# Performance work log

Measured on AMD Instinct MI355X. Metric: run time of the kernel, lower is better.

Reference implementation:

```python
import jax, jax.numpy as jnp
import numpy as np

N_NODES = 100000


def _mean_aggregate(h, src, dst, inv_deg):
    # gather source-node features per edge, scatter-add into dst, divide by in-degree
    summed = jax.ops.segment_sum(h[src], dst, num_segments=N_NODES)  # [N, d]
    return summed * inv_deg[:, None]


def setup_inputs() -> dict:
    key = jax.random.key(0)
    ks = jax.random.split(key, 6)
    n_edges, d = 640000, 128
    h = jax.random.normal(ks[0], (N_NODES, d), dtype=jnp.float32)
    src = jax.random.randint(ks[1], (n_edges,), 0, N_NODES, dtype=jnp.int64)
    dst = jax.random.randint(ks[2], (n_edges,), 0, N_NODES, dtype=jnp.int64)
    W_self = jax.random.normal(ks[3], (3, d, d), dtype=jnp.float32) / np.sqrt(d)
    W_neigh = jax.random.normal(ks[4], (3, d, d), dtype=jnp.float32) / np.sqrt(d)
    b = jnp.zeros((3, d), dtype=jnp.float32)
    return {"h": h, "src": src, "dst": dst, "W_self": W_self, "W_neigh": W_neigh, "b": b}


def reference(h, src, dst, W_self, W_neigh, b):
    # in-degree with clamp to 1 (isolated nodes aggregate to zero)
    deg = jax.ops.segment_sum(jnp.ones_like(src, dtype=h.dtype), dst, num_segments=N_NODES)
    inv_deg = 1.0 / jnp.maximum(deg, 1.0)
    n_layers = W_self.shape[0]
    for i in range(n_layers):
        neigh = _mean_aggregate(h, src, dst, inv_deg)
        h = h @ W_self[i] + neigh @ W_neigh[i] + b[i]
        if i < n_layers - 1:
            h = jax.nn.relu(h)  # dropout p=0 / eval: no-op
    return h
```

## Files before the change

kernel.cpp:

```cpp
#include <hip/hip_runtime.h>
#include <cstdint>
#include <cstddef>

#define NN 100000
#define NPAD 100032
#define D 128
#define K2 256

typedef __attribute__((ext_vector_type(8))) short bf16x8;
typedef __attribute__((ext_vector_type(4))) float f32x4;

__device__ inline float bfhi2f(unsigned int u) {
    union { unsigned int i; float f; } v; v.i = u & 0xffff0000u; return v.f;
}
__device__ inline float bflo2f(unsigned int u) {
    union { unsigned int i; float f; } v; v.i = u << 16; return v.f;
}
__device__ inline unsigned short f2bf(float f) {
    union { float f; unsigned int i; } v; v.f = f;
    unsigned int r = v.i + 0x7FFFu + ((v.i >> 16) & 1u);
    return (unsigned short)(r >> 16);
}

__global__ void k_deg(const int* __restrict__ dst, int ne, int* __restrict__ deg) {
    int e = blockIdx.x * blockDim.x + threadIdx.x;
    if (e < ne) atomicAdd(&deg[dst[e]], 1);
}

__global__ void k_chunk_reduce(const int* __restrict__ deg, int n, int* __restrict__ bsum) {
    __shared__ int s[256];
    int i = blockIdx.x * 256 + threadIdx.x;
    s[threadIdx.x] = (i < n) ? deg[i] : 0;
    __syncthreads();
    for (int off = 128; off > 0; off >>= 1) {
        if (threadIdx.x < off) s[threadIdx.x] += s[threadIdx.x + off];
        __syncthreads();
    }
    if (threadIdx.x == 0) bsum[blockIdx.x] = s[0];
}

__global__ __launch_bounds__(512) void k_scan_partials(int* __restrict__ bsum, int nb,
                                                       int* __restrict__ rowptr, int n) {
    __shared__ int s[512];
    int tid = threadIdx.x;
    int v = (tid < nb) ? bsum[tid] : 0;
    s[tid] = v;
    __syncthreads();
    for (int off = 1; off < 512; off <<= 1) {
        int t = (tid >= off) ? s[tid - off] : 0;
        __syncthreads();
        s[tid] += t;
        __syncthreads();
    }
    if (tid < nb) bsum[tid] = s[tid] - v;
    if (tid == nb - 1) rowptr[n] = s[tid];
}

__global__ void k_chunk_scan(const int* __restrict__ deg, int n, const int* __restrict__ bsum,
                             int* __restrict__ rowptr, int* __restrict__ cursor,
                             float* __restrict__ invd) {
    __shared__ int s[256];
    int tid = threadIdx.x;
    int i = blockIdx.x * 256 + tid;
    int v = (i < n) ? deg[i] : 0;
    s[tid] = v;
    __syncthreads();
    for (int off = 1; off < 256; off <<= 1) {
        int t = (tid >= off) ? s[tid - off] : 0;
        __syncthreads();
        s[tid] += t;
        __syncthreads();
    }
    if (i < n) {
        int excl = bsum[blockIdx.x] + s[tid] - v;
        rowptr[i] = excl;
        cursor[i] = excl;
        invd[i] = 1.0f / fmaxf((float)v, 1.0f);
    }
}

__global__ void k_fill(const int* __restrict__ src, const int* __restrict__ dst, int ne,
                       int* __restrict__ cursor, int* __restrict__ col) {
    int e = blockIdx.x * blockDim.x + threadIdx.x;
    if (e < ne) {
        int p = atomicAdd(&cursor[dst[e]], 1);
        col[p] = src[e];
    }
}

#define T_H   (NN * 32)
#define T_BT  (3 * 128 * K2)
#define T_Z   (NN / 4)
__global__ void k_prep(const float* __restrict__ h, const float* __restrict__ Ws,
                       const float* __restrict__ Wn, unsigned short* __restrict__ Ht,
                       unsigned short* __restrict__ Btf, int4* __restrict__ degz) {
    int t = blockIdx.x * 256 + threadIdx.x;
    if (t < T_H) {
        int row = t >> 5, c4 = (t & 31) << 2;
        float4 v = *(const float4*)(h + (size_t)row * D + c4);
        ushort4 o = make_ushort4(f2bf(v.x), f2bf(v.y), f2bf(v.z), f2bf(v.w));
        *(ushort4*)(Ht + (size_t)row * D + c4) = o;
    } else if (t < T_H + T_BT) {
        int t2 = t - T_H;
        int j = t2 & 7; int rest = t2 >> 3;
        int lane = rest & 63; rest >>= 6;
        int ks = rest & 7; rest >>= 3;
        int nf = rest & 7; int l = rest >> 3;
        int nn = nf * 16 + (lane & 15);
        int k = ks * 32 + (lane >> 4) * 8 + j;
        float v = (k < D) ? Ws[(size_t)l * D * D + (size_t)k * D + nn]
                          : Wn[(size_t)l * D * D + (size_t)(k - D) * D + nn];
        Btf[t2] = f2bf(v);
    } else {
        int t3 = t - T_H - T_BT;
        if (t3 < T_Z) degz[t3] = make_int4(0, 0, 0, 0);
    }
}

__global__ __launch_bounds__(256, 3) void k_layer(const unsigned short* __restrict__ Hin,
                                                  const unsigned short* __restrict__ Btf,
                                                  const float* __restrict__ bias,
                                                  const int* __restrict__ rowptr,
                                                  const int* __restrict__ col,
                                                  const float* __restrict__ invd,
                                                  unsigned short* __restrict__ Hout,
                                                  float* __restrict__ outf,
                                                  int relu) {
    __shared__ unsigned short Ah[64 * 128];
    __shared__ unsigned short An[64 * 128];
    int wid = threadIdx.x >> 6;
    int lane = threadIdx.x & 63;
    int g = lane >> 4;
    int lane16 = lane & 15;
    int m0 = blockIdx.x * 64;

#pragma unroll
    for (int i = 0; i < 4; ++i) {
        int chunk = wid * 4 + i;
        int o = chunk * 1024 + lane * 16;
        int row = o >> 8;
        int cb = o & 255;
        int scb = cb ^ ((row & 7) << 4);
        const unsigned short* gsrc = Hin + (size_t)(m0 + row) * D + (scb >> 1);
        __builtin_amdgcn_global_load_lds(
            (const __attribute__((address_space(1))) unsigned int*)gsrc,
            (__attribute__((address_space(3))) unsigned int*)((char*)Ah + chunk * 1024),
            16, 0, 0);
    }

    int coff = lane16 * 8;
    for (int c = 0; c < 4; ++c) {
        int row = wid * 16 + c * 4 + g;
        int node = m0 + row;
        int e0 = 0, n = 0;
        float inv = 0.f;
        if (node < NN) {
            e0 = rowptr[node];
            n = rowptr[node + 1] - e0;
            inv = invd[node];
        }
        float a0 = 0.f, a1 = 0.f, a2 = 0.f, a3 = 0.f, a4 = 0.f, a5 = 0.f, a6 = 0.f, a7 = 0.f;
        for (int base = 0; base < n; base += 16) {
            int rem = n - base;
            int lim = rem < 16 ? rem : 16;
            int cidx = lane16 < rem ? lane16 : rem - 1;
            int cv = col[e0 + base + cidx];
            for (int j = 0; j < lim; j += 8) {
                uint4 u[8];
#pragma unroll
                for (int k = 0; k < 8; ++k) {
                    int ee = j + k;
                    int eidx = ee < lim ? ee : lim - 1;
                    int si = __shfl(cv, (g << 4) + eidx, 64);
                    u[k] = *(const uint4*)(Hin + (size_t)si * D + coff);
                }
#pragma unroll
                for (int k = 0; k < 8; ++k) {
                    bool live = (j + k) < lim;
                    unsigned int ux = live ? u[k].x : 0u, uy = live ? u[k].y : 0u;
                    unsigned int uz = live ? u[k].z : 0u, uw = live ? u[k].w : 0u;
                    a0 += bflo2f(ux); a1 += bfhi2f(ux);
                    a2 += bflo2f(uy); a3 += bfhi2f(uy);
                    a4 += bflo2f(uz); a5 += bfhi2f(uz);
                    a6 += bflo2f(uw); a7 += bfhi2f(uw);
                }
            }
        }
        uint4 o;
        o.x = ((unsigned int)f2bf(a1 * inv) << 16) | f2bf(a0 * inv);
        o.y = ((unsigned int)f2bf(a3 * inv) << 16) | f2bf(a2 * inv);
        o.z = ((unsigned int)f2bf(a5 * inv) << 16) | f2bf(a4 * inv);
        o.w = ((unsigned int)f2bf(a7 * inv) << 16) | f2bf(a6 * inv);
        int bo = row * 256 + ((lane16 * 16) ^ ((row & 7) << 4));
        *(uint4*)((char*)An + bo) = o;
    }

    bf16x8 bfr[2][8];
#pragma unroll
    for (int q = 0; q < 2; ++q) {
        int nf = wid + q * 4;
#pragma unroll
        for (int ks = 0; ks < 8; ++ks)
            bfr[q][ks] = *(const bf16x8*)(Btf + (size_t)(((nf * 8 + ks) << 6) + lane) * 8);
    }

    __syncthreads();

    f32x4 acc[4][2];
#pragma unroll
    for (int mt = 0; mt < 4; ++mt)
#pragma unroll
        for (int q = 0; q < 2; ++q) acc[mt][q] = (f32x4){0.f, 0.f, 0.f, 0.f};

#pragma unroll
    for (int mt = 0; mt < 4; ++mt) {
        int row = mt * 16 + lane16;
        int swz = (row & 7) << 4;
        bf16x8 a[8];
#pragma unroll
        for (int ks = 0; ks < 8; ++ks) {
            int kb = ks * 64 + g * 16;
            const char* basep = (kb < 256) ? (const char*)Ah : (const char*)An;
            int cb2 = (kb & 255) ^ swz;
            a[ks] = *(const bf16x8*)(basep + row * 256 + cb2);
        }
#pragma unroll
        for (int ks = 0; ks < 8; ++ks) {
            acc[mt][0] = __builtin_amdgcn_mfma_f32_16x16x32_bf16(a[ks], bfr[0][ks], acc[mt][0], 0, 0, 0);
            acc[mt][1] = __builtin_amdgcn_mfma_f32_16x16x32_bf16(a[ks], bfr[1][ks], acc[mt][1], 0, 0, 0);
        }
    }

    float bv[2];
    bv[0] = bias[wid * 16 + lane16];
    bv[1] = bias[(wid + 4) * 16 + lane16];
#pragma unroll
    for (int mt = 0; mt < 4; ++mt) {
#pragma unroll
        for (int q = 0; q < 2; ++q) {
            int colc = (wid + q * 4) * 16 + lane16;
#pragma unroll
            for (int i = 0; i < 4; ++i) {
                int row = m0 + mt * 16 + g * 4 + i;
                if (row >= NN) continue;
                float v = acc[mt][q][i] + bv[q];
                if (relu) v = fmaxf(v, 0.f);
                if (outf) outf[(size_t)row * D + colc] = v;
                else Hout[(size_t)row * D + colc] = f2bf(v);
            }
        }
    }
}

extern "C" void kernel_launch(void* const* d_in, const int* in_sizes, int n_in,
                              void* d_out, int out_size, void* d_ws, size_t ws_size,
                              hipStream_t stream) {
    const float* h = (const float*)d_in[0];
    const int* src = (const int*)d_in[1];
    const int* dst = (const int*)d_in[2];
    const float* Ws = (const float*)d_in[3];
    const float* Wn = (const float*)d_in[4];
    const float* b = (const float*)d_in[5];
    float* out = (float*)d_out;
    int ne = in_sizes[1];

    char* ws = (char*)d_ws;
    unsigned short* HtA = (unsigned short*)ws; ws += (size_t)NPAD * D * sizeof(unsigned short);
    unsigned short* HtB = (unsigned short*)ws; ws += (size_t)NPAD * D * sizeof(unsigned short);
    int* col = (int*)ws;    ws += (size_t)ne * sizeof(int);
    unsigned short* Btf = (unsigned short*)ws; ws += (size_t)3 * 128 * K2 * sizeof(unsigned short);
    int* deg = (int*)ws;    ws += (size_t)NN * sizeof(int);
    int* cursor = (int*)ws; ws += (size_t)NN * sizeof(int);
    int* rowptr = (int*)ws; ws += ((size_t)(NN + 1) * sizeof(int) + 15) / 16 * 16;
    int* bsum = (int*)ws;   ws += 512 * sizeof(int);
    float* invd = (float*)ws;

    int nchunk = (NN + 255) / 256;
    int nprep = (T_H + T_BT + T_Z + 255) / 256;
    k_prep<<<nprep, 256, 0, stream>>>(h, Ws, Wn, HtA, Btf, (int4*)deg);
    k_deg<<<(ne + 255) / 256, 256, 0, stream>>>(dst, ne, deg);
    k_chunk_reduce<<<nchunk, 256, 0, stream>>>(deg, NN, bsum);
    k_scan_partials<<<1, 512, 0, stream>>>(bsum, nchunk, rowptr, NN);
    k_chunk_scan<<<nchunk, 256, 0, stream>>>(deg, NN, bsum, rowptr, cursor, invd);
    k_fill<<<(ne + 255) / 256, 256, 0, stream>>>(src, dst, ne, cursor, col);

    int ngrid = NPAD / 64;
    k_layer<<<ngrid, 256, 0, stream>>>(HtA, Btf, b, rowptr, col, invd,
                                       HtB, nullptr, 1);
    k_layer<<<ngrid, 256, 0, stream>>>(HtB, Btf + (size_t)1 * 128 * K2, b + 1 * D,
                                       rowptr, col, invd, HtA, nullptr, 1);
    k_layer<<<ngrid, 256, 0, stream>>>(HtA, Btf + (size_t)2 * 128 * K2, b + 2 * D,
                                       rowptr, col, invd, nullptr, out, 0);
}
```

Measured before the change: 221.2 us.

## Fuse CSR build into one cooperative kernel and stage layer epilogue through LDS

Replaces the five CSR-construction kernels (degree count, chunk reduce, partial scan, chunk scan, fill) with a single cooperative kernel of 391 blocks that separates phases with grid-wide syncs, removing launch gaps and the degree-zeroing pass inside k_prep. The layer epilogue now writes results into swizzled LDS and then emits coalesced 16-byte global stores, replacing scattered 2- or 4-byte per-lane stores. In exchange, the CSR build runs on fewer threads with several grid barriers, and the epilogue adds a block barrier and LDS round trip.

```diff
diff --git a/kernel.cpp b/kernel.cpp
--- a/kernel.cpp
+++ b/kernel.cpp
@@ -1,11 +1,15 @@
 #include <hip/hip_runtime.h>
+#include <hip/hip_cooperative_groups.h>
 #include <cstdint>
 #include <cstddef>
+
+namespace cg = cooperative_groups;
 
 #define NN 100000
 #define NPAD 100032
 #define D 128
 #define K2 256
+#define NBLK 391
 
 typedef __attribute__((ext_vector_type(8))) short bf16x8;
 typedef __attribute__((ext_vector_type(4))) float f32x4;
@@ -22,78 +26,11 @@
     return (unsigned short)(r >> 16);
 }
 
-__global__ void k_deg(const int* __restrict__ dst, int ne, int* __restrict__ deg) {
-    int e = blockIdx.x * blockDim.x + threadIdx.x;
-    if (e < ne) atomicAdd(&deg[dst[e]], 1);
-}
-
-__global__ void k_chunk_reduce(const int* __restrict__ deg, int n, int* __restrict__ bsum) {
-    __shared__ int s[256];
-    int i = blockIdx.x * 256 + threadIdx.x;
-    s[threadIdx.x] = (i < n) ? deg[i] : 0;
-    __syncthreads();
-    for (int off = 128; off > 0; off >>= 1) {
-        if (threadIdx.x < off) s[threadIdx.x] += s[threadIdx.x + off];
-        __syncthreads();
-    }
-    if (threadIdx.x == 0) bsum[blockIdx.x] = s[0];
-}
-
-__global__ __launch_bounds__(512) void k_scan_partials(int* __restrict__ bsum, int nb,
-                                                       int* __restrict__ rowptr, int n) {
-    __shared__ int s[512];
-    int tid = threadIdx.x;
-    int v = (tid < nb) ? bsum[tid] : 0;
-    s[tid] = v;
-    __syncthreads();
-    for (int off = 1; off < 512; off <<= 1) {
-        int t = (tid >= off) ? s[tid - off] : 0;
-        __syncthreads();
-        s[tid] += t;
-        __syncthreads();
-    }
-    if (tid < nb) bsum[tid] = s[tid] - v;
-    if (tid == nb - 1) rowptr[n] = s[tid];
-}
-
-__global__ void k_chunk_scan(const int* __restrict__ deg, int n, const int* __restrict__ bsum,
-                             int* __restrict__ rowptr, int* __restrict__ cursor,
-                             float* __restrict__ invd) {
-    __shared__ int s[256];
-    int tid = threadIdx.x;
-    int i = blockIdx.x * 256 + tid;
-    int v = (i < n) ? deg[i] : 0;
-    s[tid] = v;
-    __syncthreads();
-    for (int off = 1; off < 256; off <<= 1) {
-        int t = (tid >= off) ? s[tid - off] : 0;
-        __syncthreads();
-        s[tid] += t;
-        __syncthreads();
-    }
-    if (i < n) {
-        int excl = bsum[blockIdx.x] + s[tid] - v;
-        rowptr[i] = excl;
-        cursor[i] = excl;
-        invd[i] = 1.0f / fmaxf((float)v, 1.0f);
-    }
-}
-
-__global__ void k_fill(const int* __restrict__ src, const int* __restrict__ dst, int ne,
-                       int* __restrict__ cursor, int* __restrict__ col) {
-    int e = blockIdx.x * blockDim.x + threadIdx.x;
-    if (e < ne) {
-        int p = atomicAdd(&cursor[dst[e]], 1);
-        col[p] = src[e];
-    }
-}
-
 #define T_H   (NN * 32)
 #define T_BT  (3 * 128 * K2)
-#define T_Z   (NN / 4)
 __global__ void k_prep(const float* __restrict__ h, const float* __restrict__ Ws,
                        const float* __restrict__ Wn, unsigned short* __restrict__ Ht,
-                       unsigned short* __restrict__ Btf, int4* __restrict__ degz) {
+                       unsigned short* __restrict__ Btf) {
     int t = blockIdx.x * 256 + threadIdx.x;
     if (t < T_H) {
         int row = t >> 5, c4 = (t & 31) << 2;
@@ -111,9 +48,64 @@
         float v = (k < D) ? Ws[(size_t)l * D * D + (size_t)k * D + nn]
                           : Wn[(size_t)l * D * D + (size_t)(k - D) * D + nn];
         Btf[t2] = f2bf(v);
-    } else {
-        int t3 = t - T_H - T_BT;
-        if (t3 < T_Z) degz[t3] = make_int4(0, 0, 0, 0);
+    }
+}
+
+__global__ __launch_bounds__(256) void k_csr(const int* __restrict__ src,
+                                             const int* __restrict__ dst, int ne,
+                                             int* __restrict__ deg, int* __restrict__ bsum,
+                                             int* __restrict__ rowptr, int* __restrict__ cursor,
+                                             float* __restrict__ invd, int* __restrict__ col) {
+    cg::grid_group grid = cg::this_grid();
+    __shared__ int s[256];
+    __shared__ int p[512];
+    int tid = threadIdx.x;
+    int gtid = blockIdx.x * 256 + tid;
+    const int nthreads = NBLK * 256;
+
+    for (int i = gtid; i < NN; i += nthreads) deg[i] = 0;
+    grid.sync();
+    for (int e = gtid; e < ne; e += nthreads) atomicAdd(&deg[dst[e]], 1);
+    grid.sync();
+    int i = gtid;
+    int v = (i < NN) ? deg[i] : 0;
+    s[tid] = v;
+    __syncthreads();
+    for (int off = 1; off < 256; off <<= 1) {
+        int t = (tid >= off) ? s[tid - off] : 0;
+        __syncthreads();
+        s[tid] += t;
+        __syncthreads();
+    }
+    if (tid == 255) bsum[blockIdx.x] = s[255];
+    grid.sync();
+    if (blockIdx.x == 0) {
+        int a0 = (tid < NBLK) ? bsum[tid] : 0;
+        int a1 = (tid + 256 < NBLK) ? bsum[tid + 256] : 0;
+        p[tid] = a0; p[tid + 256] = a1;
+        __syncthreads();
+        for (int off = 1; off < 512; off <<= 1) {
+            int t0 = (tid >= off) ? p[tid - off] : 0;
+            int t1 = (tid + 256 >= off) ? p[tid + 256 - off] : 0;
+            __syncthreads();
+            p[tid] += t0; p[tid + 256] += t1;
+            __syncthreads();
+        }
+        if (tid < NBLK) bsum[tid] = p[tid] - a0;
+        if (tid + 256 < NBLK) bsum[tid + 256] = p[tid + 256] - a1;
+        if (tid == 0) rowptr[NN] = p[NBLK - 1];
+    }
+    grid.sync();
+    if (i < NN) {
+        int excl = bsum[blockIdx.x] + s[tid] - v;
+        rowptr[i] = excl;
+        cursor[i] = excl;
+        invd[i] = 1.0f / fmaxf((float)v, 1.0f);
+    }
+    grid.sync();
+    for (int e = gtid; e < ne; e += nthreads) {
+        int pos = atomicAdd(&cursor[dst[e]], 1);
+        col[pos] = src[e];
     }
 }
 
@@ -126,10 +118,12 @@
                                                   unsigned short* __restrict__ Hout,
                                                   float* __restrict__ outf,
                                                   int relu) {
-    __shared__ unsigned short Ah[64 * 128];
-    __shared__ unsigned short An[64 * 128];
-    int wid = threadIdx.x >> 6;
-    int lane = threadIdx.x & 63;
+    __shared__ unsigned short smem[64 * 256];
+    unsigned short* Ah = smem;
+    unsigned short* An = smem + 64 * 128;
+    int tid = threadIdx.x;
+    int wid = tid >> 6;
+    int lane = tid & 63;
     int g = lane >> 4;
     int lane16 = lane & 15;
     int m0 = blockIdx.x * 64;
@@ -234,20 +228,58 @@
     float bv[2];
     bv[0] = bias[wid * 16 + lane16];
     bv[1] = bias[(wid + 4) * 16 + lane16];
-#pragma unroll
-    for (int mt = 0; mt < 4; ++mt) {
-#pragma unroll
-        for (int q = 0; q < 2; ++q) {
-            int colc = (wid + q * 4) * 16 + lane16;
-#pragma unroll
-            for (int i = 0; i < 4; ++i) {
-                int row = m0 + mt * 16 + g * 4 + i;
-                if (row >= NN) continue;
-                float v = acc[mt][q][i] + bv[q];
-                if (relu) v = fmaxf(v, 0.f);
-                if (outf) outf[(size_t)row * D + colc] = v;
-                else Hout[(size_t)row * D + colc] = f2bf(v);
+    __syncthreads();
+
+    if (outf) {
+#pragma unroll
+        for (int mt = 0; mt < 4; ++mt) {
+#pragma unroll
+            for (int q = 0; q < 2; ++q) {
+#pragma unroll
+                for (int i = 0; i < 4; ++i) {
+                    int row = mt * 16 + g * 4 + i;
+                    float v = acc[mt][q][i] + bv[q];
+                    int colb = ((wid + q * 4) * 16 + lane16) * 4;
+                    int bo = row * 512 + (colb ^ ((row & 7) << 4));
+                    *(float*)((char*)smem + bo) = v;
+                }
             }
+        }
+        __syncthreads();
+        int row = tid >> 2, seg = tid & 3;
+        if (m0 + row < NN) {
+            int swz = (row & 7) << 4;
+#pragma unroll
+            for (int j = 0; j < 8; ++j) {
+                int lb = seg * 128 + j * 16;
+                uint4 val = *(const uint4*)((char*)smem + row * 512 + (lb ^ swz));
+                *(uint4*)((char*)outf + (size_t)(m0 + row) * 512 + lb) = val;
+            }
+        }
+    } else {
+#pragma unroll
+        for (int mt = 0; mt < 4; ++mt) {
+#pragma unroll
+            for (int q = 0; q < 2; ++q) {
+#pragma unroll
+                for (int i = 0; i < 4; ++i) {
+                    int row = mt * 16 + g * 4 + i;
+                    float v = acc[mt][q][i] + bv[q];
+                    if (relu) v = fmaxf(v, 0.f);
+                    int colb = ((wid + q * 4) * 16 + lane16) * 2;
+                    int bo = row * 256 + (colb ^ ((row & 7) << 4));
+                    *(unsigned short*)((char*)smem + bo) = f2bf(v);
+                }
+            }
+        }
+        __syncthreads();
+        int row = tid >> 2, seg = tid & 3;
+        int swz = (row & 7) << 4;
+#pragma unroll
+        for (int j = 0; j < 4; ++j) {
+            int lb = seg * 64 + j * 16;
+            uint4 val = *(const uint4*)((char*)smem + row * 256 + (lb ^ swz));
+            *(uint4*)((char*)Hout + (size_t)(m0 + row) * 256 + lb) = val;
         }
     }
 }
@@ -275,14 +307,12 @@
     int* bsum = (int*)ws;   ws += 512 * sizeof(int);
     float* invd = (float*)ws;
 
-    int nchunk = (NN + 255) / 256;
-    int nprep = (T_H + T_BT + T_Z + 255) / 256;
-    k_prep<<<nprep, 256, 0, stream>>>(h, Ws, Wn, HtA, Btf, (int4*)deg);
-    k_deg<<<(ne + 255) / 256, 256, 0, stream>>>(dst, ne, deg);
-    k_chunk_reduce<<<nchunk, 256, 0, stream>>>(deg, NN, bsum);
-    k_scan_partials<<<1, 512, 0, stream>>>(bsum, nchunk, rowptr, NN);
-    k_chunk_scan<<<nchunk, 256, 0, stream>>>(deg, NN, bsum, rowptr, cursor, invd);
-    k_fill<<<(ne + 255) / 256, 256, 0, stream>>>(src, dst, ne, cursor, col);
+    int nprep = (T_H + T_BT + 255) / 256;
+    k_prep<<<nprep, 256, 0, stream>>>(h, Ws, Wn, HtA, Btf);
+
+    void* csr_args[] = {(void*)&src, (void*)&dst, (void*)&ne, (void*)&deg, (void*)&bsum,
+                        (void*)&rowptr, (void*)&cursor, (void*)&invd, (void*)&col};
+    hipLaunchCooperativeKernel((const void*)k_csr, dim3(NBLK), dim3(256), csr_args, 0, stream);
 
     int ngrid = NPAD / 64;
     k_layer<<<ngrid, 256, 0, stream>>>(HtA, Btf, b, rowptr, col, invd,
```

Result: slower. 429.3 us (+94.1%).
